# Kernel tuning notes

Measured on AMD Instinct MI355X. Metric: run time of the kernel, lower is better.

Reference implementation:

```python
import jax, jax.numpy as jnp
import numpy as np

EPS = 1e-12  # F.normalize eps
TEMP = 0.03


def _l2norm(x):
    # torch F.normalize: x / max(||x||, eps)
    n = jnp.sqrt(jnp.sum(x * x, axis=-1, keepdims=True))
    return x / jnp.maximum(n, EPS)


def setup_inputs() -> dict:
    key = jax.random.key(0)
    ks = jax.random.split(key, 8)
    B, C, H, W = 8, 256, 64, 64
    M = 2024
    Ch = C // 4
    s = 1.0 / np.sqrt(C)
    return {
        "feats": jax.random.normal(ks[0], (B, C, H, W), jnp.float32),
        "fg_memory": jax.random.normal(ks[1], (M, C), jnp.float32) * s,
        "bg_memory": jax.random.normal(ks[2], (M, C), jnp.float32) * s,
        "w1_fg": jax.random.normal(ks[3], (C, Ch), jnp.float32) * s,
        "b1_fg": jnp.zeros((Ch,), jnp.float32),
        "w2_fg": jax.random.normal(ks[4], (Ch, 1), jnp.float32) * (1.0 / np.sqrt(Ch)),
        "b2_fg": jnp.zeros((1,), jnp.float32),
        "w1_bg": jax.random.normal(ks[5], (C, Ch), jnp.float32) * s,
        "b1_bg": jnp.zeros((Ch,), jnp.float32),
        "w2_bg": jax.random.normal(ks[6], (Ch, 1), jnp.float32) * (1.0 / np.sqrt(Ch)),
        "b2_bg": jnp.zeros((1,), jnp.float32),
    }


def _gate(x, w1, b1, w2, b2):
    h = jax.nn.relu(x @ w1 + b1)
    return jax.nn.sigmoid(h @ w2 + b2)  # [N,1]


def reference(feats, fg_memory, bg_memory, w1_fg, b1_fg, w2_fg, b2_fg,
              w1_bg, b1_bg, w2_bg, b2_bg):
    B, C, H, W = feats.shape
    x = jnp.transpose(feats, (0, 2, 3, 1)).reshape(-1, C)  # [N,C]
    xn = _l2norm(x)
    fgn = _l2norm(fg_memory)  # [M,C]
    bgn = _l2norm(bg_memory)

    attn_fg = jax.nn.softmax((xn @ fgn.T) / TEMP, axis=1)  # [N,M]
    mem_fg = attn_fg @ fgn                                  # [N,C]
    attn_bg = jax.nn.softmax((xn @ bgn.T) / TEMP, axis=1)
    mem_bg = attn_bg @ bgn

    g_fg = _gate(xn, w1_fg, b1_fg, w2_fg, b2_fg)
    g_bg = _gate(xn, w1_bg, b1_bg, w2_bg, b2_bg)

    fused = xn + g_fg * mem_fg - g_bg * mem_bg
    return jnp.transpose(fused.reshape(B, H, W, C), (0, 3, 1, 2))
```

## Files before the change

### kernel.cpp

```cpp
#include <hip/hip_runtime.h>
#include <math.h>

#define B_   8
#define C_   256
#define HW_  4096
#define N_   32768
#define M_   2024
#define MP_  2048
#define CH_  64
#define NCHUNK (MP_ / 64)
#define INV_TEMP 33.333333333333336f
#define NEPS 1e-12f

typedef __attribute__((ext_vector_type(8))) short short8;
typedef __attribute__((ext_vector_type(4))) float floatx4;

__device__ __forceinline__ float wred64(float s) {
#pragma unroll
  for (int off = 32; off > 0; off >>= 1) s += __shfl_xor(s, off, 64);
  return s;
}

__device__ __forceinline__ unsigned short f2bf(float f) {
  union { float f; unsigned u; } v; v.f = f;
  unsigned r = v.u + 0x7FFFu + ((v.u >> 16) & 1u);
  return (unsigned short)(r >> 16);
}
__device__ __forceinline__ float bf2f(unsigned short b) {
  union { unsigned u; float f; } v; v.u = ((unsigned)b) << 16; return v.f;
}

__device__ __forceinline__ void barrier_lds_only() {
  asm volatile("s_waitcnt lgkmcnt(0)\n\ts_barrier" ::: "memory");
}

__device__ __forceinline__ void async_copy16(const unsigned short* gsrc,
                                             unsigned short* lds) {
  __builtin_amdgcn_global_load_lds(
      (const __attribute__((address_space(1))) void*)gsrc,
      (__attribute__((address_space(3))) void*)lds, 16, 0, 0);
}

__global__ __launch_bounds__(256) void norm_mem_kernel(
    const float* __restrict__ fg, const float* __restrict__ bg,
    unsigned short* __restrict__ fgS, unsigned short* __restrict__ bgS,
    unsigned short* __restrict__ fgT, unsigned short* __restrict__ bgT) {
  __shared__ unsigned short tile[64][258];
  int bid = blockIdx.x;
  const float* src; unsigned short *ms, *mt; int r0;
  if (bid < 32) { src = fg; ms = fgS; mt = fgT; r0 = bid * 64; }
  else          { src = bg; ms = bgS; mt = bgT; r0 = (bid - 32) * 64; }
  int t = threadIdx.x;
  int rr = t >> 2, c4 = t & 3;
  int row = r0 + rr;
  int chunk = r0 >> 6;
  float v[64];
  float s = 0.f;
  if (row < M_) {
    const float4* p = (const float4*)(src + (size_t)row * C_ + c4 * 64);
#pragma unroll
    for (int i = 0; i < 16; ++i) {
      float4 q = p[i];
      v[i * 4 + 0] = q.x; v[i * 4 + 1] = q.y; v[i * 4 + 2] = q.z; v[i * 4 + 3] = q.w;
      s += q.x * q.x + q.y * q.y + q.z * q.z + q.w * q.w;
    }
  } else {
#pragma unroll
    for (int i = 0; i < 64; ++i) v[i] = 0.f;
  }
  s += __shfl_xor(s, 1, 64);
  s += __shfl_xor(s, 2, 64);
  float inv = (row < M_) ? 1.0f / fmaxf(sqrtf(s), NEPS) : 0.f;
#pragma unroll
  for (int i = 0; i < 16; ++i) {
    int c = c4 * 64 + i * 4;
    ushort4 o;
    o.x = f2bf(v[i * 4 + 0] * inv); o.y = f2bf(v[i * 4 + 1] * inv);
    o.z = f2bf(v[i * 4 + 2] * inv); o.w = f2bf(v[i * 4 + 3] * inv);
    int unit = (chunk * 32 + (c >> 5) * 4 + ((c >> 3) & 3)) * 64 + rr;
    *(ushort4*)&ms[(size_t)unit * 8 + (c & 7)] = o;
    *(ushort4*)&tile[rr][c] = o;
  }
  __syncthreads();
  int m = t & 63, cw = t >> 6;
#pragma unroll 8
  for (int j = 0; j < 64; ++j) {
    int c = cw * 64 + j;
    mt[(size_t)c * MP_ + r0 + m] = tile[m][c];
  }
}

__global__ __launch_bounds__(256) void prep_x_kernel(
    const float* __restrict__ feats, float* __restrict__ invn,
    unsigned short* __restrict__ xnb) {
  __shared__ unsigned short tileb[256][66];
  __shared__ float part[4][64];
  __shared__ float invs[64];
  int t = threadIdx.x, hwl = t & 63, cw = t >> 6;
  int n0 = blockIdx.x * 64;
  int b = n0 >> 12, hw0 = n0 & 4095;
  const float* p = feats + (size_t)b * C_ * HW_ + hw0 + hwl;
  float s = 0.f;
#pragma unroll 8
  for (int i = 0; i < 64; ++i) {
    int c = cw * 64 + i;
    float v = p[(size_t)c * HW_];
    s += v * v;
    tileb[c][hwl] = f2bf(v);
  }
  part[cw][hwl] = s;
  __syncthreads();
  if (t < 64) {
    float tot = part[0][t] + part[1][t] + part[2][t] + part[3][t];
    float inv = 1.0f / fmaxf(sqrtf(tot), NEPS);
    invn[n0 + t] = inv;
    invs[t] = inv;
  }
  __syncthreads();
  int px = t >> 2, q = t & 3;
  float iv = invs[px];
  unsigned short* xp = xnb + (size_t)(n0 + px) * C_;
#pragma unroll
  for (int blk = 0; blk < 8; ++blk) {
    int cb = blk * 4 + q;
    short8 o;
#pragma unroll
    for (int j = 0; j < 8; ++j)
      o[j] = (short)f2bf(bf2f(tileb[cb * 8 + j][px]) * iv);
    *(short8*)&xp[cb * 8] = o;
  }
}

__global__ __launch_bounds__(256) void gate_kernel(
    const unsigned short* __restrict__ xnb,
    const float* __restrict__ w1f, const float* __restrict__ b1f,
    const float* __restrict__ w2f, const float* __restrict__ b2f,
    const float* __restrict__ w1b, const float* __restrict__ b1b,
    const float* __restrict__ w2b, const float* __restrict__ b2b,
    float* __restrict__ gf, float* __restrict__ gb) {
  __shared__ float xr[16][C_];
  int t = threadIdx.x, w = t >> 6, lane = t & 63;
  int n0 = blockIdx.x * 16;
#pragma unroll
  for (int pp = 0; pp < 4; ++pp) {
    int px = w * 4 + pp;
    ushort4 u = *(const ushort4*)&xnb[(size_t)(n0 + px) * C_ + lane * 4];
    xr[px][lane * 4 + 0] = bf2f(u.x);
    xr[px][lane * 4 + 1] = bf2f(u.y);
    xr[px][lane * 4 + 2] = bf2f(u.z);
    xr[px][lane * 4 + 3] = bf2f(u.w);
  }
  __syncthreads();
  float hf[4], hb[4];
#pragma unroll
  for (int pp = 0; pp < 4; ++pp) { hf[pp] = b1f[lane]; hb[pp] = b1b[lane]; }
#pragma unroll 4
  for (int c = 0; c < C_; ++c) {
    float wf = w1f[c * CH_ + lane];
    float wb = w1b[c * CH_ + lane];
#pragma unroll
    for (int pp = 0; pp < 4; ++pp) {
      float x = xr[w * 4 + pp][c];
      hf[pp] += x * wf;
      hb[pp] += x * wb;
    }
  }
  float b2fv = b2f[0], b2bv = b2b[0];
#pragma unroll
  for (int pp = 0; pp < 4; ++pp) {
    float sf = fmaxf(hf[pp], 0.f) * w2f[lane];
    float sb = fmaxf(hb[pp], 0.f) * w2b[lane];
    sf = wred64(sf);
    sb = wred64(sb);
    if (lane == 0) {
      gf[n0 + w * 4 + pp] = 1.f / (1.f + __expf(-(sf + b2fv)));
      gb[n0 + w * 4 + pp] = 1.f / (1.f + __expf(-(sb + b2bv)));
    }
  }
}

__device__ __forceinline__ void stage_chunk(const unsigned short* memS, int mc,
                                            unsigned short* mtile, int w, int l) {
  const unsigned short* src = memS + (size_t)mc * 16384;
#pragma unroll
  for (int it = 0; it < 4; ++it) {
    int seg = (it * 8 + w) * 512;
    async_copy16(src + seg + l * 8, mtile + seg);
  }
}

__global__ __launch_bounds__(512, 4) void flash_fused_kernel(
    const unsigned short* __restrict__ xnb,
    const unsigned short* __restrict__ fgS, const unsigned short* __restrict__ fgT,
    const unsigned short* __restrict__ bgS, const unsigned short* __restrict__ bgT,
    const float* __restrict__ gf, const float* __restrict__ gb,
    const float* __restrict__ feats, const float* __restrict__ invn,
    float* __restrict__ out) {
  __shared__ __align__(16) char smem[49664];
  unsigned short* mtile = (unsigned short*)smem;
  unsigned short* Pbuf0 = (unsigned short*)(smem + 32768);
  unsigned short* Pbuf1 = (unsigned short*)(smem + 40960);
  float* rowsum = (float*)(smem + 49152);
  float* comb   = (float*)(smem + 49408);
  float* trans  = (float*)smem;

  int t = threadIdx.x;
  int w = t >> 6, l = t & 63;
  int lm = l & 15, quad = l >> 4;
  int rg = w & 3, mh = w >> 2;
  int row0 = blockIdx.x * 64;

  short8 afrag[8];
  {
    const unsigned short* ap = xnb + (size_t)(row0 + 16 * rg + lm) * C_ + quad * 8;
#pragma unroll
    for (int kb = 0; kb < 8; ++kb)
      afrag[kb] = *(const short8*)(ap + kb * 32);
  }

  int bb = row0 >> 12, hw0 = row0 & 4095;
  float iv = invn[row0 + l];
  size_t ob = (size_t)bb * (size_t)C_ * HW_ + hw0 + l;

#pragma unroll 1
  for (int pass = 0; pass < 2; ++pass) {
    const unsigned short* memS  = pass ? bgS : fgS;
    const unsigned short* membT = pass ? bgT : fgT;
    const float* gp = pass ? gb : gf;

    floatx4 accO[4][2];
#pragma unroll
    for (int rt = 0; rt < 4; ++rt)
#pragma unroll
      for (int ct = 0; ct < 2; ++ct) accO[rt][ct] = (floatx4){0.f, 0.f, 0.f, 0.f};
    float rs[4] = {0.f, 0.f, 0.f, 0.f};
    if (t < 64) rowsum[t] = 0.f;

    stage_chunk(memS, 0, mtile, w, l);

#pragma unroll 1
    for (int mc = 0; mc < NCHUNK; ++mc) {
      __syncthreads();

      short8 bfT[2][2];
#pragma unroll
      for (int ct = 0; ct < 2; ++ct) {
        const unsigned short* tp =
            membT + (size_t)(w * 32 + ct * 16 + lm) * MP_ + mc * 64 + quad * 8;
        bfT[ct][0] = *(const short8*)(tp);
        bfT[ct][1] = *(const short8*)(tp + 32);
      }

      floatx4 accS[2];
      accS[0] = (floatx4){0.f, 0.f, 0.f, 0.f};
      accS[1] = (floatx4){0.f, 0.f, 0.f, 0.f};
#pragma unroll
      for (int mt2 = 0; mt2 < 2; ++mt2) {
        int mrow = mh * 32 + mt2 * 16 + lm;
#pragma unroll
        for (int kb = 0; kb < 8; ++kb) {
          short8 bf = *(const short8*)&mtile[(size_t)(((kb * 4 + quad) * 64) + mrow) * 8];
          accS[mt2] = __builtin_amdgcn_mfma_f32_16x16x32_bf16(afrag[kb], bf, accS[mt2], 0, 0, 0);
        }
      }

      unsigned short* P = (mc & 1) ? Pbuf1 : Pbuf0;
#pragma unroll
      for (int mt2 = 0; mt2 < 2; ++mt2) {
        int m = mh * 32 + mt2 * 16 + lm;
        bool valid = (mc * 64 + m < M_);
        int g = mh * 4 + mt2 * 2 + (lm >> 3);
#pragma unroll
        for (int r = 0; r < 4; ++r) {
          float pv = valid ? __expf(accS[mt2][r] * INV_TEMP) : 0.f;
          unsigned short pb = f2bf(pv);
          rs[r] += bf2f(pb);
          P[(g * 64 + 16 * rg + quad * 4 + r) * 8 + (lm & 7)] = pb;
        }
      }
      barrier_lds_only();

      if (mc + 1 < NCHUNK) stage_chunk(memS, mc + 1, mtile, w, l);

#pragma unroll
      for (int rt = 0; rt < 4; ++rt) {
        short8 pf0 = *(const short8*)&P[(size_t)((0 + quad) * 64 + rt * 16 + lm) * 8];
        short8 pf1 = *(const short8*)&P[(size_t)((4 + quad) * 64 + rt * 16 + lm) * 8];
#pragma unroll
        for (int ct = 0; ct < 2; ++ct) {
          accO[rt][ct] = __builtin_amdgcn_mfma_f32_16x16x32_bf16(pf0, bfT[ct][0], accO[rt][ct], 0, 0, 0);
          accO[rt][ct] = __builtin_amdgcn_mfma_f32_16x16x32_bf16(pf1, bfT[ct][1], accO[rt][ct], 0, 0, 0);
        }
      }
    }

#pragma unroll
    for (int off = 1; off < 16; off <<= 1)
#pragma unroll
      for (int r = 0; r < 4; ++r) rs[r] += __shfl_xor(rs[r], off, 64);
    if (lm == 0) {
#pragma unroll
      for (int r = 0; r < 4; ++r) atomicAdd(&rowsum[16 * rg + quad * 4 + r], rs[r]);
    }
    __syncthreads();
    if (t < 64) comb[t] = gp[row0 + t] / rowsum[t];
    __syncthreads();

#pragma unroll 1
    for (int cg2 = 0; cg2 < 4; ++cg2) {
      if ((w >> 1) == cg2) {
#pragma unroll
        for (int rt = 0; rt < 4; ++rt)
#pragma unroll
          for (int r = 0; r < 4; ++r) {
            float cf = comb[16 * rt + quad * 4 + r];
#pragma unroll
            for (int ct = 0; ct < 2; ++ct)
              trans[(16 * rt + quad * 4 + r) * 67 + (w & 1) * 32 + ct * 16 + lm] =
                  cf * accO[rt][ct][r];
          }
      }
      __syncthreads();
      if (pass == 0) {
#pragma unroll
        for (int i = 0; i < 8; ++i) {
          int cl = w * 8 + i;
          int cg = cg2 * 64 + cl;
          out[ob + (size_t)cg * HW_] = trans[l * 67 + cl];
        }
      } else {
#pragma unroll
        for (int i = 0; i < 8; ++i) {
          int cl = w * 8 + i;
          int cg = cg2 * 64 + cl;
          size_t a = ob + (size_t)cg * HW_;
          out[a] = feats[a] * iv + out[a] - trans[l * 67 + cl];
        }
      }
      __syncthreads();
    }
  }
}

extern "C" void kernel_launch(void* const* d_in, const int* in_sizes, int n_in,
                              void* d_out, int out_size, void* d_ws, size_t ws_size,
                              hipStream_t stream) {
  const float* feats = (const float*)d_in[0];
  const float* fg    = (const float*)d_in[1];
  const float* bg    = (const float*)d_in[2];
  const float* w1f   = (const float*)d_in[3];
  const float* b1f   = (const float*)d_in[4];
  const float* w2f   = (const float*)d_in[5];
  const float* b2f   = (const float*)d_in[6];
  const float* w1b   = (const float*)d_in[7];
  const float* b1b   = (const float*)d_in[8];
  const float* w2b   = (const float*)d_in[9];
  const float* b2b   = (const float*)d_in[10];
  float* out = (float*)d_out;

  char* ws = (char*)d_ws;
  unsigned short* xnb = (unsigned short*)ws;
  unsigned short* fgS = xnb + (size_t)N_ * C_;
  unsigned short* bgS = fgS + (size_t)MP_ * C_;
  unsigned short* fgT = bgS + (size_t)MP_ * C_;
  unsigned short* bgT = fgT + (size_t)C_ * MP_;
  float* gf   = (float*)(bgT + (size_t)C_ * MP_);
  float* gb   = gf + N_;
  float* invn = gb + N_;

  norm_mem_kernel<<<64, 256, 0, stream>>>(fg, bg, fgS, bgS, fgT, bgT);
  prep_x_kernel<<<N_ / 64, 256, 0, stream>>>(feats, invn, xnb);
  gate_kernel<<<N_ / 16, 256, 0, stream>>>(xnb, w1f, b1f, w2f, b2f,
                                           w1b, b1b, w2b, b2b, gf, gb);
  flash_fused_kernel<<<N_ / 64, 512, 0, stream>>>(
      xnb, fgS, fgT, bgS, bgT, gf, gb, feats, invn, out);
}
```

Before: 344.9 us.

## Fuse gate MLP into flash kernel via MFMA and drop LDS staging of memory tiles

Removes the separate gate kernel: the W1 weights are pre-packed to bf16 MFMA fragment layout in an extra block of the memory-normalisation kernel, and the flash kernel computes both gate values with MFMAs from its already-loaded x fragments. It also stops staging memory chunks into LDS with async global-to-LDS copies and reads B fragments straight from global memory (L2), which shrinks LDS use and removes one barrier per chunk. The row sums now accumulate unrounded fp32 probabilities instead of bf16-rounded ones. The cost is more global and L2 read traffic per block and a slight change in numerics, in exchange for fewer launches and possibly higher occupancy.

```diff
diff --git a/kernel.cpp b/kernel.cpp
--- a/kernel.cpp
+++ b/kernel.cpp
@@ -34,23 +34,39 @@
   asm volatile("s_waitcnt lgkmcnt(0)\n\ts_barrier" ::: "memory");
 }
 
-__device__ __forceinline__ void async_copy16(const unsigned short* gsrc,
-                                             unsigned short* lds) {
-  __builtin_amdgcn_global_load_lds(
-      (const __attribute__((address_space(1))) void*)gsrc,
-      (__attribute__((address_space(3))) void*)lds, 16, 0, 0);
-}
-
 __global__ __launch_bounds__(256) void norm_mem_kernel(
     const float* __restrict__ fg, const float* __restrict__ bg,
     unsigned short* __restrict__ fgS, unsigned short* __restrict__ bgS,
-    unsigned short* __restrict__ fgT, unsigned short* __restrict__ bgT) {
+    unsigned short* __restrict__ fgT, unsigned short* __restrict__ bgT,
+    const float* __restrict__ w1f, const float* __restrict__ b1f,
+    const float* __restrict__ w2f, const float* __restrict__ b2f,
+    const float* __restrict__ w1b, const float* __restrict__ b1b,
+    const float* __restrict__ w2b, const float* __restrict__ b2b,
+    unsigned short* __restrict__ wgB, float* __restrict__ gmeta) {
+  int bid = blockIdx.x;
+  int t = threadIdx.x;
+  if (bid >= 64) {
+    for (int u = t; u < 4096; u += 256) {
+      int gate = u >> 11, ct = (u >> 9) & 3, kb = (u >> 6) & 7, l = u & 63;
+      const float* w1 = gate ? w1b : w1f;
+      int h = ct * 16 + (l & 15);
+      int cbase = kb * 32 + (l >> 4) * 8;
+#pragma unroll
+      for (int j = 0; j < 8; ++j)
+        wgB[(size_t)u * 8 + j] = f2bf(w1[(size_t)(cbase + j) * CH_ + h]);
+    }
+    if (t < 128) {
+      int gate = t >> 6, h = t & 63;
+      gmeta[t]       = gate ? b1b[h] : b1f[h];
+      gmeta[128 + t] = gate ? w2b[h] : w2f[h];
+    }
+    if (t < 2) gmeta[256 + t] = t ? b2b[0] : b2f[0];
+    return;
+  }
   __shared__ unsigned short tile[64][258];
-  int bid = blockIdx.x;
   const float* src; unsigned short *ms, *mt; int r0;
   if (bid < 32) { src = fg; ms = fgS; mt = fgT; r0 = bid * 64; }
   else          { src = bg; ms = bgS; mt = bgT; r0 = (bid - 32) * 64; }
-  int t = threadIdx.x;
   int rr = t >> 2, c4 = t & 3;
   int row = r0 + rr;
   int chunk = r0 >> 6;
@@ -131,78 +147,20 @@
   }
 }
 
-__global__ __launch_bounds__(256) void gate_kernel(
-    const unsigned short* __restrict__ xnb,
-    const float* __restrict__ w1f, const float* __restrict__ b1f,
-    const float* __restrict__ w2f, const float* __restrict__ b2f,
-    const float* __restrict__ w1b, const float* __restrict__ b1b,
-    const float* __restrict__ w2b, const float* __restrict__ b2b,
-    float* __restrict__ gf, float* __restrict__ gb) {
-  __shared__ float xr[16][C_];
-  int t = threadIdx.x, w = t >> 6, lane = t & 63;
-  int n0 = blockIdx.x * 16;
-#pragma unroll
-  for (int pp = 0; pp < 4; ++pp) {
-    int px = w * 4 + pp;
-    ushort4 u = *(const ushort4*)&xnb[(size_t)(n0 + px) * C_ + lane * 4];
-    xr[px][lane * 4 + 0] = bf2f(u.x);
-    xr[px][lane * 4 + 1] = bf2f(u.y);
-    xr[px][lane * 4 + 2] = bf2f(u.z);
-    xr[px][lane * 4 + 3] = bf2f(u.w);
-  }
-  __syncthreads();
-  float hf[4], hb[4];
-#pragma unroll
-  for (int pp = 0; pp < 4; ++pp) { hf[pp] = b1f[lane]; hb[pp] = b1b[lane]; }
-#pragma unroll 4
-  for (int c = 0; c < C_; ++c) {
-    float wf = w1f[c * CH_ + lane];
-    float wb = w1b[c * CH_ + lane];
-#pragma unroll
-    for (int pp = 0; pp < 4; ++pp) {
-      float x = xr[w * 4 + pp][c];
-      hf[pp] += x * wf;
-      hb[pp] += x * wb;
-    }
-  }
-  float b2fv = b2f[0], b2bv = b2b[0];
-#pragma unroll
-  for (int pp = 0; pp < 4; ++pp) {
-    float sf = fmaxf(hf[pp], 0.f) * w2f[lane];
-    float sb = fmaxf(hb[pp], 0.f) * w2b[lane];
-    sf = wred64(sf);
-    sb = wred64(sb);
-    if (lane == 0) {
-      gf[n0 + w * 4 + pp] = 1.f / (1.f + __expf(-(sf + b2fv)));
-      gb[n0 + w * 4 + pp] = 1.f / (1.f + __expf(-(sb + b2bv)));
-    }
-  }
-}
-
-__device__ __forceinline__ void stage_chunk(const unsigned short* memS, int mc,
-                                            unsigned short* mtile, int w, int l) {
-  const unsigned short* src = memS + (size_t)mc * 16384;
-#pragma unroll
-  for (int it = 0; it < 4; ++it) {
-    int seg = (it * 8 + w) * 512;
-    async_copy16(src + seg + l * 8, mtile + seg);
-  }
-}
-
 __global__ __launch_bounds__(512, 4) void flash_fused_kernel(
     const unsigned short* __restrict__ xnb,
     const unsigned short* __restrict__ fgS, const unsigned short* __restrict__ fgT,
     const unsigned short* __restrict__ bgS, const unsigned short* __restrict__ bgT,
-    const float* __restrict__ gf, const float* __restrict__ gb,
+    const unsigned short* __restrict__ wgB, const float* __restrict__ gmeta,
     const float* __restrict__ feats, const float* __restrict__ invn,
     float* __restrict__ out) {
-  __shared__ __align__(16) char smem[49664];
-  unsigned short* mtile = (unsigned short*)smem;
-  unsigned short* Pbuf0 = (unsigned short*)(smem + 32768);
-  unsigned short* Pbuf1 = (unsigned short*)(smem + 40960);
-  float* rowsum = (float*)(smem + 49152);
-  float* comb   = (float*)(smem + 49408);
+  __shared__ __align__(16) char smem[18176];
+  unsigned short* Pbuf0 = (unsigned short*)smem;
+  unsigned short* Pbuf1 = (unsigned short*)(smem + 8192);
   float* trans  = (float*)smem;
+  float* rowsum = (float*)(smem + 17152);
+  float* comb   = (float*)(smem + 17408);
+  float* gbuf   = (float*)(smem + 17664);
 
   int t = threadIdx.x;
   int w = t >> 6, l = t & 63;
@@ -218,6 +176,39 @@
       afrag[kb] = *(const short8*)(ap + kb * 32);
   }
 
+  {
+    floatx4 accH[4];
+#pragma unroll
+    for (int ct = 0; ct < 4; ++ct) accH[ct] = (floatx4){0.f, 0.f, 0.f, 0.f};
+#pragma unroll
+    for (int ct = 0; ct < 4; ++ct)
+#pragma unroll
+      for (int kb = 0; kb < 8; ++kb) {
+        short8 wf = *(const short8*)&wgB[(size_t)((((mh * 4 + ct) * 8) + kb) * 64 + l) * 8];
+        accH[ct] = __builtin_amdgcn_mfma_f32_16x16x32_bf16(afrag[kb], wf, accH[ct], 0, 0, 0);
+      }
+    float part[4] = {0.f, 0.f, 0.f, 0.f};
+#pragma unroll
+    for (int ct = 0; ct < 4; ++ct) {
+      float b1v = gmeta[mh * 64 + ct * 16 + lm];
+      float w2v = gmeta[128 + mh * 64 + ct * 16 + lm];
+#pragma unroll
+      for (int r = 0; r < 4; ++r)
+        part[r] += fmaxf(accH[ct][r] + b1v, 0.f) * w2v;
+    }
+#pragma unroll
+    for (int off = 1; off < 16; off <<= 1)
+#pragma unroll
+      for (int r = 0; r < 4; ++r) part[r] += __shfl_xor(part[r], off, 64);
+    float b2v = gmeta[256 + mh];
+    if (lm == 0) {
+#pragma unroll
+      for (int r = 0; r < 4; ++r)
+        gbuf[mh * 64 + 16 * rg + quad * 4 + r] =
+            1.f / (1.f + __expf(-(part[r] + b2v)));
+    }
+  }
+
   int bb = row0 >> 12, hw0 = row0 & 4095;
   float iv = invn[row0 + l];
   size_t ob = (size_t)bb * (size_t)C_ * HW_ + hw0 + l;
@@ -226,7 +217,6 @@
   for (int pass = 0; pass < 2; ++pass) {
     const unsigned short* memS  = pass ? bgS : fgS;
     const unsigned short* membT = pass ? bgT : fgT;
-    const float* gp = pass ? gb : gf;
 
     floatx4 accO[4][2];
 #pragma unroll
@@ -236,12 +226,8 @@
     float rs[4] = {0.f, 0.f, 0.f, 0.f};
     if (t < 64) rowsum[t] = 0.f;
 
-    stage_chunk(memS, 0, mtile, w, l);
-
 #pragma unroll 1
     for (int mc = 0; mc < NCHUNK; ++mc) {
-      __syncthreads();
-
       short8 bfT[2][2];
 #pragma unroll
       for (int ct = 0; ct < 2; ++ct) {
@@ -254,13 +240,16 @@
       floatx4 accS[2];
       accS[0] = (floatx4){0.f, 0.f, 0.f, 0.f};
       accS[1] = (floatx4){0.f, 0.f, 0.f, 0.f};
-#pragma unroll
-      for (int mt2 = 0; mt2 < 2; ++mt2) {
-        int mrow = mh * 32 + mt2 * 16 + lm;
-#pragma unroll
-        for (int kb = 0; kb < 8; ++kb) {
-          short8 bf = *(const short8*)&mtile[(size_t)(((kb * 4 + quad) * 64) + mrow) * 8];
-          accS[mt2] = __builtin_amdgcn_mfma_f32_16x16x32_bf16(afrag[kb], bf, accS[mt2], 0, 0, 0);
+      {
+        const unsigned short* sp = memS + (size_t)mc * 16384;
+#pragma unroll
+        for (int mt2 = 0; mt2 < 2; ++mt2) {
+          int mrow = mh * 32 + mt2 * 16 + lm;
+#pragma unroll
+          for (int kb = 0; kb < 8; ++kb) {
+            short8 bf = *(const short8*)&sp[(size_t)((kb * 4 + quad) * 64 + mrow) * 8];
+            accS[mt2] = __builtin_amdgcn_mfma_f32_16x16x32_bf16(afrag[kb], bf, accS[mt2], 0, 0, 0);
+          }
         }
       }
 
@@ -269,18 +258,15 @@
       for (int mt2 = 0; mt2 < 2; ++mt2) {
         int m = mh * 32 + mt2 * 16 + lm;
         bool valid = (mc * 64 + m < M_);
-        int g = mh * 4 + mt2 * 2 + (lm >> 3);
+        int g = m >> 3;
 #pragma unroll
         for (int r = 0; r < 4; ++r) {
           float pv = valid ? __expf(accS[mt2][r] * INV_TEMP) : 0.f;
-          unsigned short pb = f2bf(pv);
-          rs[r] += bf2f(pb);
-          P[(g * 64 + 16 * rg + quad * 4 + r) * 8 + (lm & 7)] = pb;
+          rs[r] += pv;
+          P[(size_t)(g * 64 + 16 * rg + quad * 4 + r) * 8 + (m & 7)] = f2bf(pv);
         }
       }
       barrier_lds_only();
-
-      if (mc + 1 < NCHUNK) stage_chunk(memS, mc + 1, mtile, w, l);
 
 #pragma unroll
       for (int rt = 0; rt < 4; ++rt) {
@@ -303,7 +289,7 @@
       for (int r = 0; r < 4; ++r) atomicAdd(&rowsum[16 * rg + quad * 4 + r], rs[r]);
     }
     __syncthreads();
-    if (t < 64) comb[t] = gp[row0 + t] / rowsum[t];
+    if (t < 64) comb[t] = gbuf[pass * 64 + t] / rowsum[t];
     __syncthreads();
 
 #pragma unroll 1
@@ -364,14 +350,14 @@
   unsigned short* bgS = fgS + (size_t)MP_ * C_;
   unsigned short* fgT = bgS + (size_t)MP_ * C_;
   unsigned short* bgT = fgT + (size_t)C_ * MP_;
-  float* gf   = (float*)(bgT + (size_t)C_ * MP_);
-  float* gb   = gf + N_;
-  float* invn = gb + N_;
-
-  norm_mem_kernel<<<64, 256, 0, stream>>>(fg, bg, fgS, bgS, fgT, bgT);
+  unsigned short* wgB = bgT + (size_t)C_ * MP_;
+  float* gmeta = (float*)(wgB + 2 * C_ * CH_);
+  float* invn  = gmeta + 272;
+
+  norm_mem_kernel<<<65, 256, 0, stream>>>(fg, bg, fgS, bgS, fgT, bgT,
+                                          w1f, b1f, w2f, b2f,
+                                          w1b, b1b, w2b, b2b, wgB, gmeta);
   prep_x_kernel<<<N_ / 64, 256, 0, stream>>>(feats, invn, xnb);
-  gate_kernel<<<N_ / 16, 256, 0, stream>>>(xnb, w1f, b1f, w2f, b2f,
-                                           w1b, b1b, w2b, b2b, gf, gb);
   flash_fused_kernel<<<N_ / 64, 512, 0, stream>>>(
-      xnb, fgS, fgT, bgS, bgT, gf, gb, feats, invn, out);
-}
+      xnb, fgS, fgT, bgS, bgT, wgB, gmeta, feats, invn, out);
+}
```

Measured after the change: 479.1 us. +38.9%, slower.
